# Performance work log

Hardware: AMD Instinct MI355X
Metric: run time of the kernel (lower is better)

The kernel has to match this reference:

```python
import jax, jax.numpy as jnp
import numpy as np

N_NODES = 50000
N_EDGES = 1200000
IN_DIM = 256
OUT_DIM = 64
SLOPE = 0.2


def setup_inputs() -> dict:
    key = jax.random.key(0)
    k1, k2, k3, k4, k5 = jax.random.split(key, 5)
    h = jax.random.normal(k1, (N_NODES, IN_DIM), dtype=jnp.float32)
    # xavier_normal-ish scale for the linear weights
    W_fc = jax.random.normal(k2, (OUT_DIM, IN_DIM), dtype=jnp.float32) * (2.0 / (IN_DIM + OUT_DIM)) ** 0.5
    W_attn = jax.random.normal(k3, (1, 2 * OUT_DIM), dtype=jnp.float32) * (2.0 / (2 * OUT_DIM + 1)) ** 0.5
    src = jax.random.randint(k4, (N_EDGES,), 0, N_NODES, dtype=jnp.int32)
    dst = jax.random.randint(k5, (N_EDGES,), 0, N_NODES, dtype=jnp.int32)
    return {"h": h, "W_fc": W_fc, "W_attn": W_attn, "src": src, "dst": dst}


def reference(h, W_fc, W_attn, src, dst):
    # node transform: z = fc(h)                      [N, D]
    z = h @ W_fc.T
    # split attn weight so we never materialize the [E, 2D] concat
    a = W_attn[0]
    a_src, a_dst = a[:OUT_DIM], a[OUT_DIM:]
    s_src = z @ a_src            # [N]
    s_dst = z @ a_dst            # [N]
    # per-edge score: leaky_relu(attn_fc([z_src, z_dst]))
    e = jax.nn.leaky_relu(s_src[src] + s_dst[dst], negative_slope=SLOPE)  # [E]
    # edge softmax over incoming edges of each dst node
    m = jax.ops.segment_max(e, dst, num_segments=N_NODES)                 # [N]
    ex = jnp.exp(e - m[dst])                                              # [E]
    denom = jax.ops.segment_sum(ex, dst, num_segments=N_NODES)            # [N]
    alpha = ex / denom[dst]                                               # [E]
    # weighted scatter-sum of source features, then ELU
    agg = jax.ops.segment_sum(alpha[:, None] * z[src], dst, num_segments=N_NODES)  # [N, D]
    return jax.nn.elu(agg)
```

## Files before the change

kernel.cpp:

```cpp
#include <hip/hip_runtime.h>
#include <math.h>

#define N_NODES 50000
#define N_EDGES 1200000
#define IN_DIM  256
#define OUT_DIM 64
#define SLOPE   0.2f
#define BNODES  64
#define NBKT    782
#define NBKT_PAD 1024
#define EPB     1024
#define NCHUNK  1172
#define BCAP    2048
#define SSTRIDE 2240

typedef unsigned int   uint;
typedef unsigned short ushort;
typedef float  f32x4  __attribute__((ext_vector_type(4)));
typedef short  short8 __attribute__((ext_vector_type(8)));

__device__ inline ushort bf16_rne(float f) {
    uint u = __float_as_uint(f);
    u += 0x7FFF + ((u >> 16) & 1);
    return (ushort)(u >> 16);
}
__device__ inline float bf16_f32(ushort s) {
    return __uint_as_float(((uint)s) << 16);
}
__device__ inline ushort f32_f16(float f) {
    _Float16 h = (_Float16)f;
    return __builtin_bit_cast(ushort, h);
}
__device__ inline float f16_f32(ushort u) {
    return (float)__builtin_bit_cast(_Float16, u);
}

__global__ __launch_bounds__(256) void k_binprep(const int* __restrict__ src,
                                                 const int* __restrict__ dst,
                                                 const float* __restrict__ Wfc,
                                                 ushort* __restrict__ Whi,
                                                 ushort* __restrict__ Wlo,
                                                 uint* __restrict__ binned,
                                                 uint* __restrict__ tab) {
    if (blockIdx.x >= NCHUNK) {
        int i = (blockIdx.x - NCHUNK) * 256 + threadIdx.x;
        float f = Wfc[i];
        ushort hi = bf16_rne(f);
        Whi[i] = hi;
        Wlo[i] = bf16_rne(f - bf16_f32(hi));
        return;
    }
    __shared__ uint staged[EPB];
    __shared__ int lhist[NBKT_PAD];
    __shared__ int lcur[NBKT_PAD];
    __shared__ int ws[256];
    const int t = threadIdx.x;
    const int c = blockIdx.x;
    const int base = c * EPB;
    const int n = min(EPB, N_EDGES - base);

    ((int4*)lhist)[t] = int4{0, 0, 0, 0};
    __syncthreads();

    int4 d4, s4;
    bool act = (4 * t < n);
    if (act) {
        d4 = ((const int4*)(dst + base))[t];
        s4 = ((const int4*)(src + base))[t];
        atomicAdd(&lhist[d4.x >> 6], 1);
        atomicAdd(&lhist[d4.y >> 6], 1);
        atomicAdd(&lhist[d4.z >> 6], 1);
        atomicAdd(&lhist[d4.w >> 6], 1);
    }
    __syncthreads();

    int4 hv = ((const int4*)lhist)[t];
    int lsum = hv.x + hv.y + hv.z + hv.w;
    ws[t] = lsum; __syncthreads();
    #pragma unroll
    for (int off = 1; off < 256; off <<= 1) {
        int x = (t >= off) ? ws[t - off] : 0;
        __syncthreads(); ws[t] += x; __syncthreads();
    }
    int excl = ws[t] - lsum;
    int p0 = excl, p1 = p0 + hv.x, p2 = p1 + hv.y, p3 = p2 + hv.z;
    lcur[4 * t]     = p0;
    lcur[4 * t + 1] = p1;
    lcur[4 * t + 2] = p2;
    lcur[4 * t + 3] = p3;
    uint4 te;
    te.x = ((uint)p0 << 11) | (uint)hv.x;
    te.y = ((uint)p1 << 11) | (uint)hv.y;
    te.z = ((uint)p2 << 11) | (uint)hv.z;
    te.w = ((uint)p3 << 11) | (uint)hv.w;
    ((uint4*)(tab + (size_t)c * NBKT_PAD))[t] = te;
    __syncthreads();

    if (act) {
        int dd[4] = {d4.x, d4.y, d4.z, d4.w};
        int ss[4] = {s4.x, s4.y, s4.z, s4.w};
        #pragma unroll
        for (int u = 0; u < 4; ++u) {
            int b = dd[u] >> 6, dl = dd[u] & 63;
            int slot = atomicAdd(&lcur[b], 1);
            staged[slot] = ((uint)dl << 16) | (uint)ss[u];
        }
    }
    __syncthreads();
    #pragma unroll
    for (int k = 0; k < EPB / 256; ++k) {
        int i = k * 256 + t;
        if (i < n) binned[base + i] = staged[i];
    }
}

__global__ __launch_bounds__(64) void k_gemm(const float* __restrict__ h,
                                             const ushort* __restrict__ Whi,
                                             const ushort* __restrict__ Wlo,
                                             const float* __restrict__ Wattn,
                                             ushort* __restrict__ zh,
                                             float* __restrict__ sS,
                                             float* __restrict__ sD) {
    const int l   = threadIdx.x;
    const int r16 = l & 15;
    const int g   = l >> 4;
    const int base = blockIdx.x * 16;

    const float*  ha = h   + (size_t)(base + r16) * IN_DIM + g * 8;
    const ushort* wh = Whi + (size_t)r16 * IN_DIM + g * 8;
    const ushort* wl = Wlo + (size_t)r16 * IN_DIM + g * 8;

    f32x4 c[4] = {{0,0,0,0},{0,0,0,0},{0,0,0,0},{0,0,0,0}};

    #pragma unroll
    for (int ks = 0; ks < 8; ++ks) {
        float4 a0 = *(const float4*)(ha + ks * 32);
        float4 a1 = *(const float4*)(ha + ks * 32 + 4);
        float af[8] = {a0.x, a0.y, a0.z, a0.w, a1.x, a1.y, a1.z, a1.w};
        short8 ahi, alo;
        #pragma unroll
        for (int i = 0; i < 8; ++i) {
            ushort hi = bf16_rne(af[i]);
            ahi[i] = (short)hi;
            alo[i] = (short)bf16_rne(af[i] - bf16_f32(hi));
        }
        #pragma unroll
        for (int n = 0; n < 4; ++n) {
            short8 bh = *(const short8*)(wh + n * 16 * IN_DIM + ks * 32);
            short8 bl = *(const short8*)(wl + n * 16 * IN_DIM + ks * 32);
            c[n] = __builtin_amdgcn_mfma_f32_16x16x32_bf16(ahi, bh, c[n], 0, 0, 0);
            c[n] = __builtin_amdgcn_mfma_f32_16x16x32_bf16(alo, bh, c[n], 0, 0, 0);
            c[n] = __builtin_amdgcn_mfma_f32_16x16x32_bf16(ahi, bl, c[n], 0, 0, 0);
        }
    }

    float aSv[4], aDv[4];
    #pragma unroll
    for (int n = 0; n < 4; ++n) {
        aSv[n] = Wattn[n * 16 + r16];
        aDv[n] = Wattn[OUT_DIM + n * 16 + r16];
    }
    #pragma unroll
    for (int r = 0; r < 4; ++r) {
        int node = base + g * 4 + r;
        float ss = 0.f, sd = 0.f;
        #pragma unroll
        for (int n = 0; n < 4; ++n) {
            float v = c[n][r];
            zh[(size_t)node * OUT_DIM + n * 16 + r16] = f32_f16(v);
            ss += v * aSv[n];
            sd += v * aDv[n];
        }
        ss += __shfl_xor(ss, 1); ss += __shfl_xor(ss, 2);
        ss += __shfl_xor(ss, 4); ss += __shfl_xor(ss, 8);
        sd += __shfl_xor(sd, 1); sd += __shfl_xor(sd, 2);
        sd += __shfl_xor(sd, 4); sd += __shfl_xor(sd, 8);
        if (r16 == 0) { sS[node] = ss; sD[node] = sd; }
    }
}

__global__ __launch_bounds__(256) void k_sort(const uint* __restrict__ binned,
                                              const uint* __restrict__ tab,
                                              const float* __restrict__ sS,
                                              const float* __restrict__ sD,
                                              uint* __restrict__ srcEx,
                                              int* __restrict__ rowptrFine,
                                              int* __restrict__ cntArr) {
    __shared__ uint lstage[BCAP];
    __shared__ uint lEdge[SSTRIDE];
    __shared__ int lhist[64], lcur[64], ws[256];
    __shared__ float ldsD[64];
    __shared__ int sPtot;
    const int b = blockIdx.x, t = threadIdx.x;
    const int node = (b << 6) + t;
    if (t < 64) {
        lhist[t] = 0;
        ldsD[t] = (node < N_NODES) ? sD[node] : 0.f;
    }
    __syncthreads();

    uint runs[5];
    int nck = 0, myCnt = 0;
    for (int c = t; c < NCHUNK; c += 256) {
        uint e = tab[(size_t)c * NBKT_PAD + b];
        runs[nck++] = e;
        myCnt += (int)(e & 0x7FF);
    }
    ws[t] = myCnt; __syncthreads();
    #pragma unroll
    for (int off = 1; off < 256; off <<= 1) {
        int x = (t >= off) ? ws[t - off] : 0;
        __syncthreads(); ws[t] += x; __syncthreads();
    }
    int pos = ws[t] - myCnt;
    int n = ws[255];
    __syncthreads();

    {
        int k = 0;
        for (int c = t; c < NCHUNK; c += 256, ++k) {
            uint e = runs[k];
            int cnt = (int)(e & 0x7FF);
            const uint* pB = binned + (size_t)c * EPB + (e >> 11);
            for (int i = 0; i < cnt; ++i) {
                uint w = pB[i];
                lstage[pos++] = w;
                atomicAdd(&lhist[w >> 16], 1);
            }
        }
    }
    __syncthreads();

    int pc = 0;
    if (t < 64) { pc = (lhist[t] + 3) & ~3; ws[t] = pc; }
    __syncthreads();
    #pragma unroll
    for (int off = 1; off < 64; off <<= 1) {
        int x = 0;
        if (t < 64 && t >= off) x = ws[t - off];
        __syncthreads();
        if (t < 64) ws[t] += x;
        __syncthreads();
    }
    if (t < 64) {
        int pexcl = ws[t] - pc;
        lcur[t] = pexcl;
        for (int j = lhist[t]; j < pc; ++j) lEdge[pexcl + j] = 0;
        if (node < N_NODES) {
            rowptrFine[node] = b * SSTRIDE + pexcl;
            cntArr[node] = pc;
        }
        if (t == 63) sPtot = ws[63];
    }
    __syncthreads();

    for (int i = t; i < n; i += 256) {
        uint w = lstage[i];
        int dl = (int)(w >> 16);
        int s  = (int)(w & 0xFFFF);
        float e = sS[s] + ldsD[dl];
        e = e > 0.f ? e : SLOPE * e;
        ushort exb = f32_f16(__expf(e));
        int slot = atomicAdd(&lcur[dl], 1);
        lEdge[slot] = ((w & 0xFFFFu) << 16) | (uint)exb;
    }
    __syncthreads();

    int ptot = sPtot;
    uint* dstp = srcEx + (size_t)b * SSTRIDE;
    for (int i = t; i < ptot; i += 256) dstp[i] = lEdge[i];
}

__global__ __launch_bounds__(256) void k_aggc(const uint2* __restrict__ zrow,
                                              const uint* __restrict__ srcEx,
                                              const int* __restrict__ rowptr,
                                              const int* __restrict__ cntArr,
                                              float* __restrict__ out) {
    int node = blockIdx.x * 4 + (threadIdx.x >> 6);
    int lane = threadIdx.x & 63;
    int q = lane >> 4, ql = lane & 15;
    int beg = rowptr[node];
    int cnt4 = cntArr[node];
    float a0 = 0.f, a1 = 0.f, a2 = 0.f, a3 = 0.f, den = 0.f;
    #pragma unroll 4
    for (int i = 0; i < cnt4; i += 4) {
        uint w = srcEx[beg + i + q];
        uint2 zp = zrow[((w >> 16) << 4) + ql];
        float ex = f16_f32((ushort)(w & 0xFFFF));
        a0 += ex * f16_f32((ushort)(zp.x & 0xFFFF));
        a1 += ex * f16_f32((ushort)(zp.x >> 16));
        a2 += ex * f16_f32((ushort)(zp.y & 0xFFFF));
        a3 += ex * f16_f32((ushort)(zp.y >> 16));
        den += ex;
    }
    a0 += __shfl_xor(a0, 16); a0 += __shfl_xor(a0, 32);
    a1 += __shfl_xor(a1, 16); a1 += __shfl_xor(a1, 32);
    a2 += __shfl_xor(a2, 16); a2 += __shfl_xor(a2, 32);
    a3 += __shfl_xor(a3, 16); a3 += __shfl_xor(a3, 32);
    den += __shfl_xor(den, 16); den += __shfl_xor(den, 32);
    if (q == 0) {
        float inv = den > 0.f ? 1.f / den : 0.f;
        float r0 = a0 * inv, r1 = a1 * inv, r2 = a2 * inv, r3 = a3 * inv;
        r0 = r0 > 0.f ? r0 : expm1f(r0);
        r1 = r1 > 0.f ? r1 : expm1f(r1);
        r2 = r2 > 0.f ? r2 : expm1f(r2);
        r3 = r3 > 0.f ? r3 : expm1f(r3);
        float4 r = make_float4(r0, r1, r2, r3);
        ((float4*)out)[(size_t)node * 16 + ql] = r;
    }
}

static inline char* alignup(char* p) {
    return (char*)(((uintptr_t)p + 63) & ~(uintptr_t)63);
}

extern "C" void kernel_launch(void* const* d_in, const int* in_sizes, int n_in,
                              void* d_out, int out_size, void* d_ws, size_t ws_size,
                              hipStream_t stream) {
    const float* h     = (const float*)d_in[0];
    const float* Wfc   = (const float*)d_in[1];
    const float* Wattn = (const float*)d_in[2];
    const int*   src   = (const int*)d_in[3];
    const int*   dst   = (const int*)d_in[4];
    float* out = (float*)d_out;

    char* p = (char*)d_ws;
    uint*   binned  = (uint*)p;   p = alignup(p + (size_t)N_EDGES * 4);
    uint*   tab     = (uint*)p;   p = alignup(p + (size_t)NCHUNK * NBKT_PAD * 4);
    uint*   srcEx   = (uint*)p;   p = alignup(p + (size_t)NBKT * SSTRIDE * 4);
    int*    rowptrF = (int*)p;    p = alignup(p + (size_t)N_NODES * 4);
    int*    cntArr  = (int*)p;    p = alignup(p + (size_t)N_NODES * 4);
    float*  sS      = (float*)p;  p = alignup(p + (size_t)N_NODES * 4);
    float*  sD      = (float*)p;  p = alignup(p + (size_t)N_NODES * 4);
    ushort* Whi     = (ushort*)p; p = alignup(p + OUT_DIM * IN_DIM * 2);
    ushort* Wlo     = (ushort*)p; p = alignup(p + OUT_DIM * IN_DIM * 2);
    ushort* zh      = (ushort*)p;

    k_binprep<<<NCHUNK + 64, 256, 0, stream>>>(src, dst, Wfc, Whi, Wlo, binned, tab);
    k_gemm<<<N_NODES / 16, 64, 0, stream>>>(h, Whi, Wlo, Wattn, zh, sS, sD);
    k_sort<<<NBKT, 256, 0, stream>>>(binned, tab, sS, sD, srcEx, rowptrF, cntArr);
    k_aggc<<<N_NODES / 4, 256, 0, stream>>>((const uint2*)zh, srcEx, rowptrF, cntArr, out);
}
```

Before: 93.69 us.

## Split z features into two halves and run aggregation twice for cache locality

The GEMM now writes the fp16 z features into two separate 32-column arrays (low and high halves), and the aggregation kernel is launched twice, once per half, with 8 edges processed concurrently per wave instead of 4. Each half-array is 3.2 MB, so the random gathers of z rows may stay in L2/LLC, while the edge list is read twice. Per-node edge padding is raised to multiples of 8 and SSTRIDE is enlarged to match. The cost is an extra kernel launch, a second pass over srcEx, and more padding edges.

```diff
diff --git a/kernel.cpp b/kernel.cpp
--- a/kernel.cpp
+++ b/kernel.cpp
@@ -12,7 +12,7 @@
 #define EPB     1024
 #define NCHUNK  1172
 #define BCAP    2048
-#define SSTRIDE 2240
+#define SSTRIDE 2496
 
 typedef unsigned int   uint;
 typedef unsigned short ushort;
@@ -118,7 +118,8 @@
                                              const ushort* __restrict__ Whi,
                                              const ushort* __restrict__ Wlo,
                                              const float* __restrict__ Wattn,
-                                             ushort* __restrict__ zh,
+                                             ushort* __restrict__ zlo,
+                                             ushort* __restrict__ zhi,
                                              float* __restrict__ sS,
                                              float* __restrict__ sD) {
     const int l   = threadIdx.x;
@@ -167,7 +168,9 @@
         #pragma unroll
         for (int n = 0; n < 4; ++n) {
             float v = c[n][r];
-            zh[(size_t)node * OUT_DIM + n * 16 + r16] = f32_f16(v);
+            ushort hv16 = f32_f16(v);
+            if (n < 2) zlo[(size_t)node * 32 + n * 16 + r16] = hv16;
+            else       zhi[(size_t)node * 32 + (n - 2) * 16 + r16] = hv16;
             ss += v * aSv[n];
             sd += v * aDv[n];
         }
@@ -232,7 +235,7 @@
     __syncthreads();
 
     int pc = 0;
-    if (t < 64) { pc = (lhist[t] + 3) & ~3; ws[t] = pc; }
+    if (t < 64) { pc = (lhist[t] + 7) & ~7; ws[t] = pc; }
     __syncthreads();
     #pragma unroll
     for (int off = 1; off < 64; off <<= 1) {
@@ -271,21 +274,22 @@
     for (int i = t; i < ptot; i += 256) dstp[i] = lEdge[i];
 }
 
-__global__ __launch_bounds__(256) void k_aggc(const uint2* __restrict__ zrow,
+__global__ __launch_bounds__(256) void k_aggc(const uint2* __restrict__ zrowH,
                                               const uint* __restrict__ srcEx,
                                               const int* __restrict__ rowptr,
                                               const int* __restrict__ cntArr,
-                                              float* __restrict__ out) {
+                                              float* __restrict__ out,
+                                              int halfSel) {
     int node = blockIdx.x * 4 + (threadIdx.x >> 6);
     int lane = threadIdx.x & 63;
-    int q = lane >> 4, ql = lane & 15;
+    int oct = lane >> 3, ql = lane & 7;
     int beg = rowptr[node];
-    int cnt4 = cntArr[node];
+    int cnt8 = cntArr[node];
     float a0 = 0.f, a1 = 0.f, a2 = 0.f, a3 = 0.f, den = 0.f;
     #pragma unroll 4
-    for (int i = 0; i < cnt4; i += 4) {
-        uint w = srcEx[beg + i + q];
-        uint2 zp = zrow[((w >> 16) << 4) + ql];
+    for (int i = 0; i < cnt8; i += 8) {
+        uint w = srcEx[beg + i + oct];
+        uint2 zp = zrowH[((w >> 16) << 3) + ql];
         float ex = f16_f32((ushort)(w & 0xFFFF));
         a0 += ex * f16_f32((ushort)(zp.x & 0xFFFF));
         a1 += ex * f16_f32((ushort)(zp.x >> 16));
@@ -293,12 +297,12 @@
         a3 += ex * f16_f32((ushort)(zp.y >> 16));
         den += ex;
     }
-    a0 += __shfl_xor(a0, 16); a0 += __shfl_xor(a0, 32);
-    a1 += __shfl_xor(a1, 16); a1 += __shfl_xor(a1, 32);
-    a2 += __shfl_xor(a2, 16); a2 += __shfl_xor(a2, 32);
-    a3 += __shfl_xor(a3, 16); a3 += __shfl_xor(a3, 32);
-    den += __shfl_xor(den, 16); den += __shfl_xor(den, 32);
-    if (q == 0) {
+    a0 += __shfl_xor(a0, 8); a0 += __shfl_xor(a0, 16); a0 += __shfl_xor(a0, 32);
+    a1 += __shfl_xor(a1, 8); a1 += __shfl_xor(a1, 16); a1 += __shfl_xor(a1, 32);
+    a2 += __shfl_xor(a2, 8); a2 += __shfl_xor(a2, 16); a2 += __shfl_xor(a2, 32);
+    a3 += __shfl_xor(a3, 8); a3 += __shfl_xor(a3, 16); a3 += __shfl_xor(a3, 32);
+    den += __shfl_xor(den, 8); den += __shfl_xor(den, 16); den += __shfl_xor(den, 32);
+    if (oct == 0) {
         float inv = den > 0.f ? 1.f / den : 0.f;
         float r0 = a0 * inv, r1 = a1 * inv, r2 = a2 * inv, r3 = a3 * inv;
         r0 = r0 > 0.f ? r0 : expm1f(r0);
@@ -306,7 +310,7 @@
         r2 = r2 > 0.f ? r2 : expm1f(r2);
         r3 = r3 > 0.f ? r3 : expm1f(r3);
         float4 r = make_float4(r0, r1, r2, r3);
-        ((float4*)out)[(size_t)node * 16 + ql] = r;
+        ((float4*)out)[(size_t)node * 16 + halfSel * 8 + ql] = r;
     }
 }
 
@@ -334,10 +338,12 @@
     float*  sD      = (float*)p;  p = alignup(p + (size_t)N_NODES * 4);
     ushort* Whi     = (ushort*)p; p = alignup(p + OUT_DIM * IN_DIM * 2);
     ushort* Wlo     = (ushort*)p; p = alignup(p + OUT_DIM * IN_DIM * 2);
-    ushort* zh      = (ushort*)p;
+    ushort* zlo     = (ushort*)p; p = alignup(p + (size_t)N_NODES * 32 * 2);
+    ushort* zhi     = (ushort*)p;
 
     k_binprep<<<NCHUNK + 64, 256, 0, stream>>>(src, dst, Wfc, Whi, Wlo, binned, tab);
-    k_gemm<<<N_NODES / 16, 64, 0, stream>>>(h, Whi, Wlo, Wattn, zh, sS, sD);
+    k_gemm<<<N_NODES / 16, 64, 0, stream>>>(h, Whi, Wlo, Wattn, zlo, zhi, sS, sD);
     k_sort<<<NBKT, 256, 0, stream>>>(binned, tab, sS, sD, srcEx, rowptrF, cntArr);
-    k_aggc<<<N_NODES / 4, 256, 0, stream>>>((const uint2*)zh, srcEx, rowptrF, cntArr, out);
-}
+    k_aggc<<<N_NODES / 4, 256, 0, stream>>>((const uint2*)zlo, srcEx, rowptrF, cntArr, out, 0);
+    k_aggc<<<N_NODES / 4, 256, 0, stream>>>((const uint2*)zhi, srcEx, rowptrF, cntArr, out, 1);
+}
```

After: 110.7 us. +18.1%, slower.

## Fuse node GEMM into edge binning kernel and drop low-bf16 activation term

Applied to the files above, without the earlier changes.

Weight splitting moves to a small separate kernel, and the node-transform GEMM runs as extra blocks of the edge-binning kernel, so binning and the GEMM execute concurrently in one launch. GEMM blocks now hold four waves covering 64 nodes, with bounds guards for the tail. The activation low-part MFMA is removed, leaving two bf16 MFMAs per tile instead of three. This cuts launches and GEMM work but lowers the precision of z, since activations are now rounded to plain bf16.

```diff
diff --git a/kernel.cpp b/kernel.cpp
--- a/kernel.cpp
+++ b/kernel.cpp
@@ -11,6 +11,7 @@
 #define NBKT_PAD 1024
 #define EPB     1024
 #define NCHUNK  1172
+#define NGEMMB  782
 #define BCAP    2048
 #define SSTRIDE 2240
 
@@ -35,21 +36,88 @@
     return (float)__builtin_bit_cast(_Float16, u);
 }
 
-__global__ __launch_bounds__(256) void k_binprep(const int* __restrict__ src,
-                                                 const int* __restrict__ dst,
-                                                 const float* __restrict__ Wfc,
-                                                 ushort* __restrict__ Whi,
-                                                 ushort* __restrict__ Wlo,
-                                                 uint* __restrict__ binned,
-                                                 uint* __restrict__ tab) {
+__global__ __launch_bounds__(256) void k_wprep(const float* __restrict__ Wfc,
+                                               ushort* __restrict__ Whi,
+                                               ushort* __restrict__ Wlo) {
+    int i = blockIdx.x * 256 + threadIdx.x;
+    if (i >= OUT_DIM * IN_DIM) return;
+    float f = Wfc[i];
+    ushort hi = bf16_rne(f);
+    Whi[i] = hi;
+    Wlo[i] = bf16_rne(f - bf16_f32(hi));
+}
+
+__global__ __launch_bounds__(256) void k_binmm(const int* __restrict__ src,
+                                               const int* __restrict__ dst,
+                                               const float* __restrict__ h,
+                                               const ushort* __restrict__ Whi,
+                                               const ushort* __restrict__ Wlo,
+                                               const float* __restrict__ Wattn,
+                                               uint* __restrict__ binned,
+                                               uint* __restrict__ tab,
+                                               ushort* __restrict__ zh,
+                                               float* __restrict__ sS,
+                                               float* __restrict__ sD) {
     if (blockIdx.x >= NCHUNK) {
-        int i = (blockIdx.x - NCHUNK) * 256 + threadIdx.x;
-        float f = Wfc[i];
-        ushort hi = bf16_rne(f);
-        Whi[i] = hi;
-        Wlo[i] = bf16_rne(f - bf16_f32(hi));
+        const int gb  = blockIdx.x - NCHUNK;
+        const int wid = threadIdx.x >> 6;
+        const int l   = threadIdx.x & 63;
+        const int r16 = l & 15;
+        const int g   = l >> 4;
+        const int base = gb * 64 + wid * 16;
+
+        int arow = base + r16;
+        if (arow >= N_NODES) arow = N_NODES - 1;
+        const float*  ha = h   + (size_t)arow * IN_DIM + g * 8;
+        const ushort* wh = Whi + (size_t)r16 * IN_DIM + g * 8;
+        const ushort* wl = Wlo + (size_t)r16 * IN_DIM + g * 8;
+
+        f32x4 c[4] = {{0,0,0,0},{0,0,0,0},{0,0,0,0},{0,0,0,0}};
+
+        #pragma unroll
+        for (int ks = 0; ks < 8; ++ks) {
+            float4 a0 = *(const float4*)(ha + ks * 32);
+            float4 a1 = *(const float4*)(ha + ks * 32 + 4);
+            float af[8] = {a0.x, a0.y, a0.z, a0.w, a1.x, a1.y, a1.z, a1.w};
+            short8 ahi;
+            #pragma unroll
+            for (int i = 0; i < 8; ++i) ahi[i] = (short)bf16_rne(af[i]);
+            #pragma unroll
+            for (int n = 0; n < 4; ++n) {
+                short8 bh = *(const short8*)(wh + n * 16 * IN_DIM + ks * 32);
+                short8 bl = *(const short8*)(wl + n * 16 * IN_DIM + ks * 32);
+                c[n] = __builtin_amdgcn_mfma_f32_16x16x32_bf16(ahi, bh, c[n], 0, 0, 0);
+                c[n] = __builtin_amdgcn_mfma_f32_16x16x32_bf16(ahi, bl, c[n], 0, 0, 0);
+            }
+        }
+
+        float aSv[4], aDv[4];
+        #pragma unroll
+        for (int n = 0; n < 4; ++n) {
+            aSv[n] = Wattn[n * 16 + r16];
+            aDv[n] = Wattn[OUT_DIM + n * 16 + r16];
+        }
+        #pragma unroll
+        for (int r = 0; r < 4; ++r) {
+            int node = base + g * 4 + r;
+            float ss = 0.f, sd = 0.f;
+            #pragma unroll
+            for (int n = 0; n < 4; ++n) {
+                float v = c[n][r];
+                if (node < N_NODES)
+                    zh[(size_t)node * OUT_DIM + n * 16 + r16] = f32_f16(v);
+                ss += v * aSv[n];
+                sd += v * aDv[n];
+            }
+            ss += __shfl_xor(ss, 1); ss += __shfl_xor(ss, 2);
+            ss += __shfl_xor(ss, 4); ss += __shfl_xor(ss, 8);
+            sd += __shfl_xor(sd, 1); sd += __shfl_xor(sd, 2);
+            sd += __shfl_xor(sd, 4); sd += __shfl_xor(sd, 8);
+            if (r16 == 0 && node < N_NODES) { sS[node] = ss; sD[node] = sd; }
+        }
         return;
     }
+
     __shared__ uint staged[EPB];
     __shared__ int lhist[NBKT_PAD];
     __shared__ int lcur[NBKT_PAD];
@@ -111,71 +179,6 @@
     for (int k = 0; k < EPB / 256; ++k) {
         int i = k * 256 + t;
         if (i < n) binned[base + i] = staged[i];
-    }
-}
-
-__global__ __launch_bounds__(64) void k_gemm(const float* __restrict__ h,
-                                             const ushort* __restrict__ Whi,
-                                             const ushort* __restrict__ Wlo,
-                                             const float* __restrict__ Wattn,
-                                             ushort* __restrict__ zh,
-                                             float* __restrict__ sS,
-                                             float* __restrict__ sD) {
-    const int l   = threadIdx.x;
-    const int r16 = l & 15;
-    const int g   = l >> 4;
-    const int base = blockIdx.x * 16;
-
-    const float*  ha = h   + (size_t)(base + r16) * IN_DIM + g * 8;
-    const ushort* wh = Whi + (size_t)r16 * IN_DIM + g * 8;
-    const ushort* wl = Wlo + (size_t)r16 * IN_DIM + g * 8;
-
-    f32x4 c[4] = {{0,0,0,0},{0,0,0,0},{0,0,0,0},{0,0,0,0}};
-
-    #pragma unroll
-    for (int ks = 0; ks < 8; ++ks) {
-        float4 a0 = *(const float4*)(ha + ks * 32);
-        float4 a1 = *(const float4*)(ha + ks * 32 + 4);
-        float af[8] = {a0.x, a0.y, a0.z, a0.w, a1.x, a1.y, a1.z, a1.w};
-        short8 ahi, alo;
-        #pragma unroll
-        for (int i = 0; i < 8; ++i) {
-            ushort hi = bf16_rne(af[i]);
-            ahi[i] = (short)hi;
-            alo[i] = (short)bf16_rne(af[i] - bf16_f32(hi));
-        }
-        #pragma unroll
-        for (int n = 0; n < 4; ++n) {
-            short8 bh = *(const short8*)(wh + n * 16 * IN_DIM + ks * 32);
-            short8 bl = *(const short8*)(wl + n * 16 * IN_DIM + ks * 32);
-            c[n] = __builtin_amdgcn_mfma_f32_16x16x32_bf16(ahi, bh, c[n], 0, 0, 0);
-            c[n] = __builtin_amdgcn_mfma_f32_16x16x32_bf16(alo, bh, c[n], 0, 0, 0);
-            c[n] = __builtin_amdgcn_mfma_f32_16x16x32_bf16(ahi, bl, c[n], 0, 0, 0);
-        }
-    }
-
-    float aSv[4], aDv[4];
-    #pragma unroll
-    for (int n = 0; n < 4; ++n) {
-        aSv[n] = Wattn[n * 16 + r16];
-        aDv[n] = Wattn[OUT_DIM + n * 16 + r16];
-    }
-    #pragma unroll
-    for (int r = 0; r < 4; ++r) {
-        int node = base + g * 4 + r;
-        float ss = 0.f, sd = 0.f;
-        #pragma unroll
-        for (int n = 0; n < 4; ++n) {
-            float v = c[n][r];
-            zh[(size_t)node * OUT_DIM + n * 16 + r16] = f32_f16(v);
-            ss += v * aSv[n];
-            sd += v * aDv[n];
-        }
-        ss += __shfl_xor(ss, 1); ss += __shfl_xor(ss, 2);
-        ss += __shfl_xor(ss, 4); ss += __shfl_xor(ss, 8);
-        sd += __shfl_xor(sd, 1); sd += __shfl_xor(sd, 2);
-        sd += __shfl_xor(sd, 4); sd += __shfl_xor(sd, 8);
-        if (r16 == 0) { sS[node] = ss; sD[node] = sd; }
     }
 }
 
@@ -336,8 +339,9 @@
     ushort* Wlo     = (ushort*)p; p = alignup(p + OUT_DIM * IN_DIM * 2);
     ushort* zh      = (ushort*)p;
 
-    k_binprep<<<NCHUNK + 64, 256, 0, stream>>>(src, dst, Wfc, Whi, Wlo, binned, tab);
-    k_gemm<<<N_NODES / 16, 64, 0, stream>>>(h, Whi, Wlo, Wattn, zh, sS, sD);
+    k_wprep<<<64, 256, 0, stream>>>(Wfc, Whi, Wlo);
+    k_binmm<<<NCHUNK + NGEMMB, 256, 0, stream>>>(src, dst, h, Whi, Wlo, Wattn,
+                                                 binned, tab, zh, sS, sD);
     k_sort<<<NBKT, 256, 0, stream>>>(binned, tab, sS, sD, srcEx, rowptrF, cntArr);
     k_aggc<<<N_NODES / 4, 256, 0, stream>>>((const uint2*)zh, srcEx, rowptrF, cntArr, out);
 }
```

New measurement: 109.6 us. +17.0%, slower.
